# Kernel optimization log

Measured on AMD Instinct MI355X. Metric: run time of the kernel, lower is better.

The kernel has to match this reference:

```python
import jax, jax.numpy as jnp
import numpy as np

INPUT_DIM = 512
EMBED_DIM = 512
N_HEAD = 8
HEAD_DIM = EMBED_DIM // N_HEAD


def setup_inputs() -> dict:
    key = jax.random.key(0)
    k0, k1, k2 = jax.random.split(key, 3)
    B, S = 2, 4096
    X = jax.random.normal(k0, (B, S, INPUT_DIM), dtype=jnp.float32)
    # xavier_uniform for Linear weights (torch weight shape [out, in])
    def xavier(k, out_f, in_f):
        bound = float(np.sqrt(6.0 / (in_f + out_f)))
        return jax.random.uniform(k, (out_f, in_f), jnp.float32, -bound, bound)
    W_qkv = xavier(k1, 3 * EMBED_DIM, INPUT_DIM)
    b_qkv = jnp.zeros((3 * EMBED_DIM,), jnp.float32)
    W_o = xavier(k2, EMBED_DIM, EMBED_DIM)
    b_o = jnp.zeros((EMBED_DIM,), jnp.float32)
    return {"X": X, "W_qkv": W_qkv, "b_qkv": b_qkv, "W_o": W_o, "b_o": b_o}


def reference(X, W_qkv, b_qkv, W_o, b_o):
    B, S, _ = X.shape
    # fused QKV projection: [B,S,3E]
    qkv = jnp.einsum("bsd,ed->bse", X, W_qkv) + b_qkv
    # [B,S,H,3*hd] -> [B,H,S,3*hd]
    qkv = qkv.reshape(B, S, N_HEAD, 3 * HEAD_DIM).transpose(0, 2, 1, 3)
    q, k, v = jnp.split(qkv, 3, axis=-1)
    scale = 1.0 / jnp.sqrt(jnp.asarray(HEAD_DIM, q.dtype))
    logits = jnp.einsum("bhqd,bhkd->bhqk", q, k) * scale  # [B,H,S,S]
    attn = jax.nn.softmax(logits, axis=-1)
    vals = jnp.einsum("bhqk,bhkd->bhqd", attn, v)
    vals = vals.transpose(0, 2, 1, 3).reshape(B, S, EMBED_DIM)
    out = jnp.einsum("bse,fe->bsf", vals, W_o) + b_o
    return out
```

## Files before the change

kernel.cpp:

```cpp
#include <hip/hip_runtime.h>

#define S_   4096
#define D_IN 512
#define E_   512
#define HD   64

typedef __attribute__((ext_vector_type(8))) short short8;
typedef __attribute__((ext_vector_type(16))) float f32x16;

#define MFMA32(a, b, c) __builtin_amdgcn_mfma_f32_32x32x16_bf16((a), (b), (c), 0, 0, 0)

__device__ __forceinline__ unsigned short f2bf(float f) {
  unsigned u = __builtin_bit_cast(unsigned, f);
  u = (u + 0x7FFFu + ((u >> 16) & 1u)) >> 16;
  return (unsigned short)u;
}

__device__ __forceinline__ unsigned cvt_pk_bf16(float lo, float hi) {
  unsigned r;
  asm("v_cvt_pk_bf16_f32 %0, %1, %2" : "=v"(r) : "v"(lo), "v"(hi));
  return r;
}

__device__ __forceinline__ f32x16 splat16(float x) {
  f32x16 v;
#pragma unroll
  for (int i = 0; i < 16; ++i) v[i] = x;
  return v;
}

__global__ __launch_bounds__(256) void cvt3(const float* __restrict__ X,
                                            const float* __restrict__ Wq,
                                            const float* __restrict__ Wo,
                                            unsigned short* __restrict__ Xb,
                                            unsigned short* __restrict__ Wqb,
                                            unsigned short* __restrict__ Wob) {
  int bid = blockIdx.x;
  const float* src;
  unsigned short* dst;
  int i;
  if (bid < 4096)      { src = X;  dst = Xb;  i = bid * 256 + threadIdx.x; }
  else if (bid < 4864) { src = Wq; dst = Wqb; i = (bid - 4096) * 256 + threadIdx.x; }
  else                 { src = Wo; dst = Wob; i = (bid - 4864) * 256 + threadIdx.x; }
  float4 v = reinterpret_cast<const float4*>(src)[i];
  ushort4 o;
  o.x = f2bf(v.x); o.y = f2bf(v.y); o.z = f2bf(v.z); o.w = f2bf(v.w);
  reinterpret_cast<ushort4*>(dst)[i] = o;
}

__global__ __launch_bounds__(256, 3) void qkv_proj(const unsigned short* __restrict__ Xb,
                                                   const unsigned short* __restrict__ Wb,
                                                   const float* __restrict__ bias,
                                                   unsigned short* __restrict__ Qb,
                                                   unsigned short* __restrict__ Kb,
                                                   unsigned short* __restrict__ Vt) {
  __shared__ unsigned short Al[128][72];
  __shared__ unsigned short Bl[128][72];
  const int tid = threadIdx.x;
  const int w = tid >> 6, l = tid & 63, h = l >> 5, r31 = l & 31;
  const int wm = w >> 1, wn = w & 1;
  const int m0 = blockIdx.x * 128, n0 = blockIdx.y * 128;
  const int sr = tid >> 1, sc = tid & 1;

  f32x16 a00 = {}, a01 = {}, a10 = {}, a11 = {};
  const unsigned short* ap = Xb + (size_t)(m0 + sr) * D_IN + sc * 32;
  const unsigned short* bp = Wb + (size_t)(n0 + sr) * D_IN + sc * 32;
  for (int k0 = 0; k0 < D_IN; k0 += 64) {
    int4 av0 = *reinterpret_cast<const int4*>(ap + k0);
    int4 av1 = *reinterpret_cast<const int4*>(ap + k0 + 8);
    int4 av2 = *reinterpret_cast<const int4*>(ap + k0 + 16);
    int4 av3 = *reinterpret_cast<const int4*>(ap + k0 + 24);
    int4 bv0 = *reinterpret_cast<const int4*>(bp + k0);
    int4 bv1 = *reinterpret_cast<const int4*>(bp + k0 + 8);
    int4 bv2 = *reinterpret_cast<const int4*>(bp + k0 + 16);
    int4 bv3 = *reinterpret_cast<const int4*>(bp + k0 + 24);
    __syncthreads();
    *reinterpret_cast<int4*>(&Al[sr][sc * 32])      = av0;
    *reinterpret_cast<int4*>(&Al[sr][sc * 32 + 8])  = av1;
    *reinterpret_cast<int4*>(&Al[sr][sc * 32 + 16]) = av2;
    *reinterpret_cast<int4*>(&Al[sr][sc * 32 + 24]) = av3;
    *reinterpret_cast<int4*>(&Bl[sr][sc * 32])      = bv0;
    *reinterpret_cast<int4*>(&Bl[sr][sc * 32 + 8])  = bv1;
    *reinterpret_cast<int4*>(&Bl[sr][sc * 32 + 16]) = bv2;
    *reinterpret_cast<int4*>(&Bl[sr][sc * 32 + 24]) = bv3;
    __syncthreads();
#pragma unroll
    for (int c = 0; c < 4; ++c) {
      short8 aA = *reinterpret_cast<const short8*>(&Al[wm * 64 + r31][c * 16 + h * 8]);
      short8 aB = *reinterpret_cast<const short8*>(&Al[wm * 64 + 32 + r31][c * 16 + h * 8]);
      short8 bA = *reinterpret_cast<const short8*>(&Bl[wn * 64 + r31][c * 16 + h * 8]);
      short8 bB = *reinterpret_cast<const short8*>(&Bl[wn * 64 + 32 + r31][c * 16 + h * 8]);
      a00 = MFMA32(aA, bA, a00);
      a01 = MFMA32(aA, bB, a01);
      a10 = MFMA32(aB, bA, a10);
      a11 = MFMA32(aB, bB, a11);
    }
  }
#pragma unroll
  for (int rb = 0; rb < 2; ++rb)
#pragma unroll
    for (int cb = 0; cb < 2; ++cb) {
      const f32x16 A = rb ? (cb ? a11 : a10) : (cb ? a01 : a00);
      int n = n0 + wn * 64 + cb * 32 + r31;
      int hh = n / 192;
      int j = n - hh * 192;
      int t3 = j >> 6;
      int d = j & 63;
      float bn = bias[n];
      int mbase0 = m0 + wm * 64 + rb * 32 + h * 4;
#pragma unroll
      for (int rq = 0; rq < 4; ++rq) {
        int mb = mbase0 + rq * 8;
        int bb = mb >> 12;
        int ssb = mb & 4095;
        int bhh = bb * 8 + hh;
        if (t3 == 0) {
#pragma unroll
          for (int i = 0; i < 4; ++i)
            Qb[((size_t)bhh * S_ + ssb + i) * HD + d] =
                f2bf((A[rq * 4 + i] + bn) * (0.125f * 1.44269504088896f));
        } else if (t3 == 1) {
#pragma unroll
          for (int i = 0; i < 4; ++i)
            Kb[((size_t)bhh * S_ + ssb + i) * HD + d] = f2bf(A[rq * 4 + i] + bn);
        } else {
          int sp = (ssb & ~12) | ((ssb & 8) >> 1) | ((ssb & 4) << 1);
          ushort4 o;
          o.x = f2bf(A[rq * 4 + 0] + bn);
          o.y = f2bf(A[rq * 4 + 1] + bn);
          o.z = f2bf(A[rq * 4 + 2] + bn);
          o.w = f2bf(A[rq * 4 + 3] + bn);
          *reinterpret_cast<ushort4*>(&Vt[((size_t)bhh * HD + d) * S_ + sp]) = o;
        }
      }
    }
}

__global__ __launch_bounds__(512, 4) void attn_fwd(const unsigned short* __restrict__ Qb,
                                                   const unsigned short* __restrict__ Kb,
                                                   const unsigned short* __restrict__ Vt,
                                                   unsigned short* __restrict__ vals) {
  __shared__ char smem[73728];
  const int tid = threadIdx.x;
  const int w = tid >> 6, l = tid & 63, h = l >> 5, r31 = l & 31;
  const int grp = w >> 2;
  const int wq = w & 3;
  const int swz = ((blockIdx.x & 7) << 6) | (blockIdx.x >> 3);
  const int bh = swz >> 5;
  const int q0 = (swz & 31) * 128;
  const int lt256 = tid & 255;
  const int sr = lt256 >> 2, sc = lt256 & 3;

  unsigned short (*Kl)[64][72] =
      reinterpret_cast<unsigned short(*)[64][72]>(smem + grp * 36864);
  unsigned short (*Vl)[64][72] =
      reinterpret_cast<unsigned short(*)[64][72]>(smem + grp * 36864 + 18432);

  const int qrow = q0 + wq * 32 + r31;
  const unsigned short* qp = Qb + ((size_t)bh * S_ + qrow) * HD + h * 8;
  short8 bq[4];
#pragma unroll
  for (int c = 0; c < 4; ++c)
    bq[c] = *reinterpret_cast<const short8*>(qp + c * 16);

  f32x16 po0 = {}, po1 = {};
  float lacc = 0.f;

  const int kvbase = grp * 2048;
  const unsigned short* kptr = Kb + ((size_t)bh * S_ + kvbase + sr) * HD + sc * 16;
  const unsigned short* vptr = Vt + ((size_t)bh * HD + sr) * S_ + kvbase + sc * 16;

  {
    int4 kA = *reinterpret_cast<const int4*>(kptr);
    int4 kB = *reinterpret_cast<const int4*>(kptr + 8);
    int4 vA = *reinterpret_cast<const int4*>(vptr);
    int4 vB = *reinterpret_cast<const int4*>(vptr + 8);
    *reinterpret_cast<int4*>(&Kl[0][sr][sc * 16])     = kA;
    *reinterpret_cast<int4*>(&Kl[0][sr][sc * 16 + 8]) = kB;
    *reinterpret_cast<int4*>(&Vl[0][sr][sc * 16])     = vA;
    *reinterpret_cast<int4*>(&Vl[0][sr][sc * 16 + 8]) = vB;
  }
  __syncthreads();

  for (int kt = 0; kt < 32; ++kt) {
    const int cur = kt & 1;
    int4 kA, kB, vA, vB;
    if (kt < 31) {
      const unsigned short* kp = kptr + (size_t)(kt + 1) * 64 * HD;
      const unsigned short* vp = vptr + (kt + 1) * 64;
      kA = *reinterpret_cast<const int4*>(kp);
      kB = *reinterpret_cast<const int4*>(kp + 8);
      vA = *reinterpret_cast<const int4*>(vp);
      vB = *reinterpret_cast<const int4*>(vp + 8);
    }

    f32x16 s0 = splat16(-16.f), s1 = splat16(-16.f);
#pragma unroll
    for (int c = 0; c < 4; ++c) {
      short8 k0 = *reinterpret_cast<const short8*>(&Kl[cur][r31][c * 16 + h * 8]);
      s0 = MFMA32(k0, bq[c], s0);
      short8 k1 = *reinterpret_cast<const short8*>(&Kl[cur][32 + r31][c * 16 + h * 8]);
      s1 = MFMA32(k1, bq[c], s1);
    }

#pragma unroll
    for (int i = 0; i < 16; ++i) {
      s0[i] = __builtin_amdgcn_exp2f(s0[i]);
      s1[i] = __builtin_amdgcn_exp2f(s1[i]);
    }
    float r0 = ((s0[0] + s0[1]) + (s0[2] + s0[3])) + ((s0[4] + s0[5]) + (s0[6] + s0[7]));
    float r1 = ((s0[8] + s0[9]) + (s0[10] + s0[11])) + ((s0[12] + s0[13]) + (s0[14] + s0[15]));
    float r2 = ((s1[0] + s1[1]) + (s1[2] + s1[3])) + ((s1[4] + s1[5]) + (s1[6] + s1[7]));
    float r3 = ((s1[8] + s1[9]) + (s1[10] + s1[11])) + ((s1[12] + s1[13]) + (s1[14] + s1[15]));
    lacc += (r0 + r1) + (r2 + r3);

#pragma unroll
    for (int c = 0; c < 4; ++c) {
      const f32x16 pp = (c < 2) ? s0 : s1;
      const int o8 = (c & 1) * 8;
      uint4 pk;
      pk.x = cvt_pk_bf16(pp[o8 + 0], pp[o8 + 1]);
      pk.y = cvt_pk_bf16(pp[o8 + 2], pp[o8 + 3]);
      pk.z = cvt_pk_bf16(pp[o8 + 4], pp[o8 + 5]);
      pk.w = cvt_pk_bf16(pp[o8 + 6], pp[o8 + 7]);
      short8 pf = __builtin_bit_cast(short8, pk);
      short8 v0 = *reinterpret_cast<const short8*>(&Vl[cur][r31][c * 16 + h * 8]);
      po0 = MFMA32(v0, pf, po0);
      short8 v1 = *reinterpret_cast<const short8*>(&Vl[cur][32 + r31][c * 16 + h * 8]);
      po1 = MFMA32(v1, pf, po1);
    }

    if (kt < 31) {
      *reinterpret_cast<int4*>(&Kl[cur ^ 1][sr][sc * 16])     = kA;
      *reinterpret_cast<int4*>(&Kl[cur ^ 1][sr][sc * 16 + 8]) = kB;
      *reinterpret_cast<int4*>(&Vl[cur ^ 1][sr][sc * 16])     = vA;
      *reinterpret_cast<int4*>(&Vl[cur ^ 1][sr][sc * 16 + 8]) = vB;
    }
    __syncthreads();
  }

  float ltp = lacc + __shfl_xor(lacc, 32);
  float* Ox = reinterpret_cast<float*>(smem);
  float* lx = reinterpret_cast<float*>(smem + 34816);
  const int qlocal = wq * 32 + r31;
  if (grp == 0) {
#pragma unroll
    for (int db = 0; db < 2; ++db) {
      const f32x16 P = db ? po1 : po0;
#pragma unroll
      for (int rq = 0; rq < 4; ++rq) {
        float4 st = {P[rq * 4 + 0], P[rq * 4 + 1], P[rq * 4 + 2], P[rq * 4 + 3]};
        *reinterpret_cast<float4*>(&Ox[qlocal * 68 + db * 32 + rq * 8 + h * 4]) = st;
      }
    }
    if (h == 0) lx[qlocal] = ltp;
  }
  __syncthreads();
  if (grp == 1) {
    float inv = 1.0f / (ltp + lx[qlocal]);
    const int b = bh >> 3, hd = bh & 7;
    unsigned short* op = vals + ((size_t)b * S_ + qrow) * E_ + hd * HD + h * 4;
#pragma unroll
    for (int db = 0; db < 2; ++db) {
      const f32x16 P = db ? po1 : po0;
#pragma unroll
      for (int rq = 0; rq < 4; ++rq) {
        float4 pv = *reinterpret_cast<const float4*>(&Ox[qlocal * 68 + db * 32 + rq * 8 + h * 4]);
        ushort4 o;
        o.x = f2bf((P[rq * 4 + 0] + pv.x) * inv);
        o.y = f2bf((P[rq * 4 + 1] + pv.y) * inv);
        o.z = f2bf((P[rq * 4 + 2] + pv.z) * inv);
        o.w = f2bf((P[rq * 4 + 3] + pv.w) * inv);
        *reinterpret_cast<ushort4*>(op + db * 32 + rq * 8) = o;
      }
    }
  }
}

__global__ __launch_bounds__(256, 4) void o_proj(const unsigned short* __restrict__ Ab,
                                                 const unsigned short* __restrict__ Wb,
                                                 const float* __restrict__ bias,
                                                 float* __restrict__ out) {
  __shared__ unsigned short Al[64][72];
  __shared__ unsigned short Bl[64][72];
  const int tid = threadIdx.x;
  const int w = tid >> 6, l = tid & 63, h = l >> 5, r31 = l & 31;
  const int wm = w >> 1, wn = w & 1;
  const int m0 = blockIdx.x * 64, n0 = blockIdx.y * 64;
  const int sr = tid >> 2, sc = tid & 3;

  f32x16 acc = {};
  const unsigned short* ap = Ab + (size_t)(m0 + sr) * E_ + sc * 16;
  const unsigned short* bp = Wb + (size_t)(n0 + sr) * E_ + sc * 16;
  for (int k0 = 0; k0 < E_; k0 += 64) {
    int4 av0 = *reinterpret_cast<const int4*>(ap + k0);
    int4 av1 = *reinterpret_cast<const int4*>(ap + k0 + 8);
    int4 bv0 = *reinterpret_cast<const int4*>(bp + k0);
    int4 bv1 = *reinterpret_cast<const int4*>(bp + k0 + 8);
    __syncthreads();
    *reinterpret_cast<int4*>(&Al[sr][sc * 16])     = av0;
    *reinterpret_cast<int4*>(&Al[sr][sc * 16 + 8]) = av1;
    *reinterpret_cast<int4*>(&Bl[sr][sc * 16])     = bv0;
    *reinterpret_cast<int4*>(&Bl[sr][sc * 16 + 8]) = bv1;
    __syncthreads();
#pragma unroll
    for (int c = 0; c < 4; ++c) {
      short8 aA = *reinterpret_cast<const short8*>(&Al[wm * 32 + r31][c * 16 + h * 8]);
      short8 bA = *reinterpret_cast<const short8*>(&Bl[wn * 32 + r31][c * 16 + h * 8]);
      acc = MFMA32(aA, bA, acc);
    }
  }
  {
    int n = n0 + wn * 32 + r31;
    float bn = bias[n];
    int mbase0 = m0 + wm * 32 + h * 4;
#pragma unroll
    for (int rq = 0; rq < 4; ++rq)
#pragma unroll
      for (int i = 0; i < 4; ++i)
        out[(size_t)(mbase0 + rq * 8 + i) * E_ + n] = acc[rq * 4 + i] + bn;
  }
}

extern "C" void kernel_launch(void* const* d_in, const int* in_sizes, int n_in,
                              void* d_out, int out_size, void* d_ws, size_t ws_size,
                              hipStream_t stream) {
  const float* X    = (const float*)d_in[0];
  const float* Wqkv = (const float*)d_in[1];
  const float* bqkv = (const float*)d_in[2];
  const float* Wo   = (const float*)d_in[3];
  const float* bo   = (const float*)d_in[4];
  float* out = (float*)d_out;

  char* ws = (char*)d_ws;
  unsigned short* Xb   = (unsigned short*)(ws);
  unsigned short* Wqb  = (unsigned short*)(ws + 8388608);
  unsigned short* Wob  = (unsigned short*)(ws + 9961472);
  unsigned short* Qb   = (unsigned short*)(ws + 10485760);
  unsigned short* Kb   = (unsigned short*)(ws + 18874368);
  unsigned short* Vt   = (unsigned short*)(ws + 27262976);
  unsigned short* vals = (unsigned short*)(ws + 35651584);

  cvt3<<<5120, 256, 0, stream>>>(X, Wqkv, Wo, Xb, Wqb, Wob);
  qkv_proj<<<dim3(64, 12), 256, 0, stream>>>(Xb, Wqb, bqkv, Qb, Kb, Vt);
  attn_fwd<<<512, 512, 0, stream>>>(Qb, Kb, Vt, vals);
  o_proj<<<dim3(128, 8), 256, 0, stream>>>(vals, Wob, bo, out);
}
```

Measured before the change: 122.0 us.

## Prefetch next K-tile in QKV GEMM and remap blocks across XCDs

The QKV projection kernel now issues the global loads for the next K-slice into registers right after the shared-memory stores, so those loads overlap with the MFMA work on the current slice. The grid is flattened to 1D and block indices are remapped so that each XCD gets a contiguous group of M-tiles, which is meant to improve L2 reuse of X tiles. This costs extra live registers, which may pressure occupancy under launch_bounds(256,3). The QKV GEMM is only one of four kernels in the forward pass.

```diff
diff --git a/kernel.cpp b/kernel.cpp
--- a/kernel.cpp
+++ b/kernel.cpp
@@ -59,21 +59,27 @@
   const int tid = threadIdx.x;
   const int w = tid >> 6, l = tid & 63, h = l >> 5, r31 = l & 31;
   const int wm = w >> 1, wn = w & 1;
-  const int m0 = blockIdx.x * 128, n0 = blockIdx.y * 128;
+  const int lin = blockIdx.x;
+  const int xcd = lin & 7;
+  const int idx = lin >> 3;
+  const int m0 = (xcd * 8 + (idx & 7)) * 128;
+  const int n0 = (idx >> 3) * 128;
   const int sr = tid >> 1, sc = tid & 1;
 
   f32x16 a00 = {}, a01 = {}, a10 = {}, a11 = {};
   const unsigned short* ap = Xb + (size_t)(m0 + sr) * D_IN + sc * 32;
   const unsigned short* bp = Wb + (size_t)(n0 + sr) * D_IN + sc * 32;
-  for (int k0 = 0; k0 < D_IN; k0 += 64) {
-    int4 av0 = *reinterpret_cast<const int4*>(ap + k0);
-    int4 av1 = *reinterpret_cast<const int4*>(ap + k0 + 8);
-    int4 av2 = *reinterpret_cast<const int4*>(ap + k0 + 16);
-    int4 av3 = *reinterpret_cast<const int4*>(ap + k0 + 24);
-    int4 bv0 = *reinterpret_cast<const int4*>(bp + k0);
-    int4 bv1 = *reinterpret_cast<const int4*>(bp + k0 + 8);
-    int4 bv2 = *reinterpret_cast<const int4*>(bp + k0 + 16);
-    int4 bv3 = *reinterpret_cast<const int4*>(bp + k0 + 24);
+
+  int4 av0 = *reinterpret_cast<const int4*>(ap);
+  int4 av1 = *reinterpret_cast<const int4*>(ap + 8);
+  int4 av2 = *reinterpret_cast<const int4*>(ap + 16);
+  int4 av3 = *reinterpret_cast<const int4*>(ap + 24);
+  int4 bv0 = *reinterpret_cast<const int4*>(bp);
+  int4 bv1 = *reinterpret_cast<const int4*>(bp + 8);
+  int4 bv2 = *reinterpret_cast<const int4*>(bp + 16);
+  int4 bv3 = *reinterpret_cast<const int4*>(bp + 24);
+
+  for (int it = 0; it < 8; ++it) {
     __syncthreads();
     *reinterpret_cast<int4*>(&Al[sr][sc * 32])      = av0;
     *reinterpret_cast<int4*>(&Al[sr][sc * 32 + 8])  = av1;
@@ -84,6 +90,19 @@
     *reinterpret_cast<int4*>(&Bl[sr][sc * 32 + 16]) = bv2;
     *reinterpret_cast<int4*>(&Bl[sr][sc * 32 + 24]) = bv3;
     __syncthreads();
+
+    if (it < 7) {
+      const int k0 = (it + 1) * 64;
+      av0 = *reinterpret_cast<const int4*>(ap + k0);
+      av1 = *reinterpret_cast<const int4*>(ap + k0 + 8);
+      av2 = *reinterpret_cast<const int4*>(ap + k0 + 16);
+      av3 = *reinterpret_cast<const int4*>(ap + k0 + 24);
+      bv0 = *reinterpret_cast<const int4*>(bp + k0);
+      bv1 = *reinterpret_cast<const int4*>(bp + k0 + 8);
+      bv2 = *reinterpret_cast<const int4*>(bp + k0 + 16);
+      bv3 = *reinterpret_cast<const int4*>(bp + k0 + 24);
+    }
+
 #pragma unroll
     for (int c = 0; c < 4; ++c) {
       short8 aA = *reinterpret_cast<const short8*>(&Al[wm * 64 + r31][c * 16 + h * 8]);
@@ -342,7 +361,7 @@
   unsigned short* vals = (unsigned short*)(ws + 35651584);
 
   cvt3<<<5120, 256, 0, stream>>>(X, Wqkv, Wo, Xb, Wqb, Wob);
-  qkv_proj<<<dim3(64, 12), 256, 0, stream>>>(Xb, Wqb, bqkv, Qb, Kb, Vt);
+  qkv_proj<<<768, 256, 0, stream>>>(Xb, Wqb, bqkv, Qb, Kb, Vt);
   attn_fwd<<<512, 512, 0, stream>>>(Qb, Kb, Vt, vals);
   o_proj<<<dim3(128, 8), 256, 0, stream>>>(vals, Wob, bo, out);
 }
```

Result: no change. 120.8 us, median of 2 (-0.9%).
